# Kernel tuning notes

Measured on AMD Instinct MI355X. Metric: run time of the kernel, lower is better.

The kernel has to match this reference:

```python
import jax, jax.numpy as jnp
from jax import lax
import numpy as np

VOCAB = 32000
EMB = 256
UNITS = 1024
STEPS = 128
START_TOKEN = 1


def setup_inputs() -> dict:
    key = jax.random.key(0)
    ks = jax.random.split(key, 7)
    B, Hf, Wf, C = 32, 8, 25, 512
    s = 0.02
    return {
        "image_encoding": jax.random.normal(ks[0], (B, Hf, Wf, C), jnp.float32),
        "embedding": jax.random.normal(ks[1], (VOCAB, EMB), jnp.float32) * s,
        "lstm_kernel": jax.random.normal(ks[2], (EMB + C, 4 * UNITS), jnp.float32) * s,
        "lstm_rec_kernel": jax.random.normal(ks[3], (UNITS, 4 * UNITS), jnp.float32) * s,
        "lstm_bias": jnp.zeros((4 * UNITS,), jnp.float32),
        "proj_w": jax.random.normal(ks[4], (UNITS, VOCAB), jnp.float32) * s,
        "proj_b": jnp.zeros((VOCAB,), jnp.float32),
    }


def _lstm_cell(x, h, c, K, R, b):
    # Keras LSTMCell: gate order i, f, c, o; sigmoid gates, tanh cell.
    z = x @ K + h @ R + b  # [B, 4*UNITS]
    zi, zf, zc, zo = jnp.split(z, 4, axis=-1)
    i = jax.nn.sigmoid(zi)
    f = jax.nn.sigmoid(zf)
    o = jax.nn.sigmoid(zo)
    c_new = f * c + i * jnp.tanh(zc)
    h_new = o * jnp.tanh(c_new)
    return h_new, c_new


def reference(image_encoding, embedding, lstm_kernel, lstm_rec_kernel, lstm_bias, proj_w, proj_b):
    B = image_encoding.shape[0]
    C = image_encoding.shape[-1]
    # flatten_image_features=False -> mean over spatial positions
    features = image_encoding.reshape(B, -1, C).mean(axis=1)  # [B, C]

    start_emb = jnp.tile(embedding[START_TOKEN][None, :], (B, 1))  # [B, EMB]
    h0 = jnp.zeros((B, UNITS), features.dtype)
    c0 = jnp.zeros((B, UNITS), features.dtype)
    key0 = jax.random.key(42)

    def step(carry, _):
        h, c, inp, key = carry
        key, sub = jax.random.split(key)
        x = jnp.concatenate([inp, features], axis=-1)  # augment(inp)
        h, c = _lstm_cell(x, h, c, lstm_kernel, lstm_rec_kernel, lstm_bias)
        logits = h @ proj_w + proj_b  # [B, VOCAB]
        samples = jax.random.categorical(sub, logits)  # [B] int
        inp = embedding[samples]  # [B, EMB]
        return (h, c, inp, key), samples

    _, samples = lax.scan(step, (h0, c0, start_emb, key0), None, length=STEPS)
    # samples: [STEPS, B] -> [B, STEPS] as in tf.transpose(convert_to_tensor(output))
    return samples.T
```

## Files before the change

kernel.cpp:

```cpp
#include <hip/hip_runtime.h>
#include <cstdint>
#include <cstddef>


#define VOCAB 32000
#define EMB 256
#define UNITS 1024
#define STEPS 128
#define BATCH 32
#define XROWS 768
#define TINYF 1.17549435e-38f

typedef uint32_t u32x16 __attribute__((ext_vector_type(16)));

__host__ __device__ __forceinline__ void tf2x32(uint32_t k0, uint32_t k1,
                                                uint32_t x0, uint32_t x1,
                                                uint32_t& o0, uint32_t& o1) {
  uint32_t ks2 = k0 ^ k1 ^ 0x1BD11BDAu;
#define TFR(r) { x0 += x1; x1 = (x1 << (r)) | (x1 >> (32 - (r))); x1 ^= x0; }
  x0 += k0; x1 += k1;
  TFR(13) TFR(15) TFR(26) TFR(6)  x0 += k1;  x1 += ks2 + 1u;
  TFR(17) TFR(29) TFR(16) TFR(24) x0 += ks2; x1 += k0 + 2u;
  TFR(13) TFR(15) TFR(26) TFR(6)  x0 += k0;  x1 += k1 + 3u;
  TFR(17) TFR(29) TFR(16) TFR(24) x0 += k1;  x1 += ks2 + 4u;
  TFR(13) TFR(15) TFR(26) TFR(6)  x0 += ks2; x1 += k0 + 5u;
#undef TFR
  o0 = x0; o1 = x1;
}

__device__ __forceinline__ void sload2_b(const float* p, u32x16& a, u32x16& b,
                                         u32x16& c, u32x16& d) {
  asm volatile("s_load_dwordx16 %0, %4, 0x0\n\t"
               "s_load_dwordx16 %1, %4, 0x40\n\t"
               "s_load_dwordx16 %2, %4, 0x80\n\t"
               "s_load_dwordx16 %3, %4, 0xc0\n\t"
               "s_waitcnt lgkmcnt(0)"
               : "=&s"(a), "=&s"(b), "=&s"(c), "=&s"(d)
               : "s"(p));
}

__device__ __forceinline__ void fma32(float* acc, float w,
                                      const u32x16& xa, const u32x16& xb) {
#pragma unroll
  for (int b = 0; b < 16; ++b)
    acc[b] = fmaf(w, __uint_as_float(xa[b]), acc[b]);
#pragma unroll
  for (int b = 0; b < 16; ++b)
    acc[b + 16] = fmaf(w, __uint_as_float(xb[b]), acc[b + 16]);
}

__global__ __launch_bounds__(256) void k_init(
    const float* __restrict__ img, const float* __restrict__ emb,
    float* __restrict__ xT, float* __restrict__ h0, float* __restrict__ cT,
    unsigned long long* __restrict__ winners, unsigned int* __restrict__ cntA,
    unsigned int* __restrict__ cntB) {
  int idx = blockIdx.x * 256 + threadIdx.x;
  if (idx < 16384) {
    int b = idx >> 9, ch = idx & 511;
    const float* p = img + (size_t)b * 102400 + ch;
    float s = 0.f;
    for (int t = 0; t < 200; ++t) s += p[(size_t)t * 512];
    xT[(size_t)(256 + ch) * 32 + b] = s / 200.0f;
  } else if (idx < 24576) {
    int i2 = idx - 16384;
    int e = i2 >> 5, b = i2 & 31;
    xT[(size_t)e * 32 + b] = emb[256 + e];
  } else if (idx < 57344) {
    h0[idx - 24576] = 0.f;
  } else if (idx < 90112) {
    cT[idx - 57344] = 0.f;
  } else if (idx < 94208) {
    winners[idx - 90112] = 0ull;
  } else if (idx < 96256) {
    cntA[idx - 94208] = 0u;
  } else if (idx < 96384) {
    cntB[idx - 96256] = 0u;
  }
}

__global__ __launch_bounds__(512) void k_lstm(
    const float* __restrict__ Km, const float* __restrict__ Rm,
    const float* __restrict__ bias, const float* __restrict__ xT,
    const float* __restrict__ hr, float* __restrict__ hw,
    float* __restrict__ cT, float* __restrict__ zpart,
    unsigned int* cntA, int t) {
  const int tid = threadIdx.x;
  const int lane = tid & 63;
  const int strip = __builtin_amdgcn_readfirstlane(tid >> 6);
  const int jt = blockIdx.x >> 3;
  const int e = blockIdx.x & 7;
  const int j = jt * 64 + lane;
  const int m = jt & 15;

  __shared__ float red[4][64][33];
  __shared__ int lastf;

  float acc[32];
#pragma unroll
  for (int b = 0; b < 32; ++b) acc[b] = 0.f;

  const int klo = e * 224 + strip * 28;
  const int khi = klo + 28;

#define WROW(g) ((g) < XROWS ? Km[(size_t)(g) * 4096 + j] \
                             : Rm[(size_t)((g) - XROWS) * 4096 + j])
  float wc0 = WROW(klo);
  float wc1 = WROW(klo + 1);
  for (int k = klo; k < khi; k += 2) {
    float wn0 = 0.f, wn1 = 0.f;
    if (k + 2 < khi) { wn0 = WROW(k + 2); wn1 = WROW(k + 3); }
    const float* xrow = (k < XROWS) ? (xT + (size_t)k * 32)
                                    : (hr + (size_t)(k - XROWS) * 32);
    u32x16 xa, xb, xc, xd;
    sload2_b(xrow, xa, xb, xc, xd);
    fma32(acc, wc0, xa, xb);
    fma32(acc, wc1, xc, xd);
    wc0 = wn0; wc1 = wn1;
  }
#undef WROW

  if (strip < 4) {
#pragma unroll
    for (int b = 0; b < 32; ++b) red[strip][lane][b] = acc[b];
  }
  __syncthreads();
  if (strip >= 4) {
#pragma unroll
    for (int b = 0; b < 32; ++b) red[strip - 4][lane][b] += acc[b];
  }
  __syncthreads();

#pragma unroll
  for (int it = 0; it < 4; ++it) {
    int idx = it * 512 + tid;
    int col = idx >> 5, b = idx & 31;
    float s = ((red[0][col][b] + red[1][col][b]) + red[2][col][b]) +
              red[3][col][b];
    zpart[((size_t)e * 4096 + jt * 64 + col) * 32 + b] = s;
  }
  __syncthreads();
  if (tid == 0) {
    __threadfence();
    unsigned int old = atomicAdd(&cntA[t * 16 + m], 1u);
    lastf = (old == 31u);
  }
  __syncthreads();

  if (lastf) {
    __threadfence();
#pragma unroll
    for (int it = 0; it < 4; ++it) {
      int idx = it * 512 + tid;
      int ul = idx >> 5, b = idx & 31;
      int u = m * 64 + ul;
      float zs[4];
#pragma unroll
      for (int g = 0; g < 4; ++g) {
        int jj = g * 1024 + u;
        const float* zp = zpart + (size_t)jj * 32 + b;
        float s = zp[0];
#pragma unroll
        for (int ee = 1; ee < 8; ++ee) s += zp[(size_t)ee * 4096 * 32];
        zs[g] = s + bias[jj];
      }
      float ig = 1.0f / (1.0f + expf(-zs[0]));
      float fg = 1.0f / (1.0f + expf(-zs[1]));
      float og = 1.0f / (1.0f + expf(-zs[3]));
      float cold = cT[(size_t)u * 32 + b];
      float cn = fg * cold + ig * tanhf(zs[2]);
      cT[(size_t)u * 32 + b] = cn;
      hw[(size_t)u * 32 + b] = og * tanhf(cn);
    }
  }
}

__global__ __launch_bounds__(512) void k_logits(
    const float* __restrict__ Pw, const float* __restrict__ pb,
    const float* __restrict__ emb, const float* __restrict__ hr,
    float* __restrict__ xT, unsigned long long* winners,
    unsigned int* cntB, int* __restrict__ out, int t, uint32_t s0,
    uint32_t s1) {
  const int tid = threadIdx.x;
  const int lane = tid & 63;
  const int strip = __builtin_amdgcn_readfirstlane(tid >> 6);
  const int v0 = blockIdx.x * 64;

  __shared__ float red[4][64][33];
  __shared__ unsigned long long wbs[32][17];
  __shared__ int samp[BATCH];
  __shared__ int lastf;

  float acc[32];
#pragma unroll
  for (int b = 0; b < 32; ++b) acc[b] = 0.f;

  {
    const float* xp = hr + (size_t)(strip * 128) * 32;
    const float* wp = Pw + (size_t)(strip * 128) * VOCAB + v0 + lane;
    float wc0 = wp[0], wc1 = wp[VOCAB], wc2 = wp[2 * VOCAB],
          wc3 = wp[3 * VOCAB];
    const float* wpp = wp + (size_t)4 * VOCAB;
    u32x16 xa, xb, xc, xd;
    for (int k = 0; k < 124; k += 4) {
      float wn0 = wpp[0], wn1 = wpp[VOCAB], wn2 = wpp[2 * VOCAB],
            wn3 = wpp[3 * VOCAB];
      wpp += (size_t)4 * VOCAB;
      sload2_b(xp, xa, xb, xc, xd); xp += 64;
      fma32(acc, wc0, xa, xb);
      fma32(acc, wc1, xc, xd);
      sload2_b(xp, xa, xb, xc, xd); xp += 64;
      fma32(acc, wc2, xa, xb);
      fma32(acc, wc3, xc, xd);
      wc0 = wn0; wc1 = wn1; wc2 = wn2; wc3 = wn3;
    }
    sload2_b(xp, xa, xb, xc, xd); xp += 64;
    fma32(acc, wc0, xa, xb);
    fma32(acc, wc1, xc, xd);
    sload2_b(xp, xa, xb, xc, xd);
    fma32(acc, wc2, xa, xb);
    fma32(acc, wc3, xc, xd);
  }

  if (strip < 4) {
#pragma unroll
    for (int b = 0; b < 32; ++b) red[strip][lane][b] = acc[b];
  }
  __syncthreads();
  if (strip >= 4) {
#pragma unroll
    for (int b = 0; b < 32; ++b) red[strip - 4][lane][b] += acc[b];
  }
  __syncthreads();

#pragma unroll
  for (int it = 0; it < 4; ++it) {
    int idx = it * 512 + tid;
    int col = idx >> 5, b = idx & 31;
    float s = ((red[0][col][b] + red[1][col][b]) + red[2][col][b]) +
              red[3][col][b] + pb[v0 + col];
    red[0][col][b] = s;
  }
  __syncthreads();

  {
    const int b = tid & 31;
    const int sub = tid >> 5;
    unsigned long long best = 0ull;
#pragma unroll
    for (int c = 0; c < 4; ++c) {
      int col = sub * 4 + c;
      int vv = v0 + col;
      float logit = red[0][col][b];
      uint32_t y0, y1;
      tf2x32(s0, s1, 0u, (uint32_t)(b * VOCAB + vv), y0, y1);
      uint32_t bits = y0 ^ y1;
      uint32_t fb = (bits >> 9) | 0x3F800000u;
      float f = __uint_as_float(fb) - 1.0f;
      float u = f + TINYF;
      u = fmaxf(TINYF, u);
      float g = -logf(-logf(u));
      float val = g + logit;
      uint32_t ub = __float_as_uint(val);
      ub = ((int)ub < 0) ? ~ub : (ub | 0x80000000u);
      unsigned long long pk =
          ((unsigned long long)ub << 32) | (uint32_t)(~(uint32_t)vv);
      if (pk > best) best = pk;
    }
    wbs[b][sub] = best;
  }
  __syncthreads();

  if (tid < 32) {
    unsigned long long best = wbs[tid][0];
#pragma unroll
    for (int s = 1; s < 16; ++s)
      best = (wbs[tid][s] > best) ? wbs[tid][s] : best;
    unsigned long long cur = winners[t * 32 + tid];
    if (best > cur) atomicMax(&winners[t * 32 + tid], best);
  }
  __syncthreads();
  if (tid == 0) {
    __threadfence();
    unsigned int old = atomicAdd(&cntB[t], 1u);
    lastf = (old == 499u);
  }
  __syncthreads();

  if (lastf) {
    __threadfence();
    if (tid < 32) {
      unsigned long long w = atomicMax(&winners[t * 32 + tid], 0ull);
      int vv = (int)(~(uint32_t)(w & 0xFFFFFFFFull));
      samp[tid] = vv;
      out[tid * STEPS + t] = vv;
    }
    __syncthreads();
#pragma unroll
    for (int it = 0; it < 16; ++it) {
      int idx = it * 512 + tid;
      int b = idx >> 8, e2 = idx & 255;
      xT[(size_t)e2 * 32 + b] = emb[(size_t)samp[b] * EMB + e2];
    }
  }
}

extern "C" void kernel_launch(void* const* d_in, const int* in_sizes, int n_in,
                              void* d_out, int out_size, void* d_ws,
                              size_t ws_size, hipStream_t stream) {
  (void)in_sizes; (void)n_in; (void)out_size; (void)ws_size;
  const float* img  = (const float*)d_in[0];
  const float* emb  = (const float*)d_in[1];
  const float* Km   = (const float*)d_in[2];
  const float* Rm   = (const float*)d_in[3];
  const float* bias = (const float*)d_in[4];
  const float* Pw   = (const float*)d_in[5];
  const float* pb   = (const float*)d_in[6];
  int* out = (int*)d_out;

  char* ws = (char*)d_ws;
  unsigned long long* winners = (unsigned long long*)(ws + 0);
  unsigned int* cntA = (unsigned int*)(ws + 32768);
  unsigned int* cntB = (unsigned int*)(ws + 40960);
  float* xT   = (float*)(ws + 49152);
  float* hb0  = (float*)(ws + 147456);
  float* hb1  = (float*)(ws + 278528);
  float* cT   = (float*)(ws + 409600);
  float* zpart = (float*)(ws + 540672);

  k_init<<<377, 256, 0, stream>>>(img, emb, xT, hb0, cT, winners, cntA, cntB);

  uint32_t k0 = 0u, k1 = 42u;
  for (int t = 0; t < STEPS; ++t) {
    uint32_t n0, n1, su0, su1;
    tf2x32(k0, k1, 0u, 0u, n0, n1);
    tf2x32(k0, k1, 0u, 1u, su0, su1);
    k0 = n0; k1 = n1;

    const float* hrd = (t & 1) ? hb1 : hb0;
    float* hwr = (t & 1) ? hb0 : hb1;
    k_lstm<<<512, 512, 0, stream>>>(Km, Rm, bias, xT, hrd, hwr, cT, zpart,
                                    cntA, t);
    k_logits<<<500, 512, 0, stream>>>(Pw, pb, emb, hwr, xT, winners, cntB,
                                      out, t, su0, su1);
  }
}
```

Baseline: 11.22 ms.

## Split logits projection K-dimension across two blocks per vocab tile with atomic handoff

```diff
diff --git a/kernel.cpp b/kernel.cpp
--- a/kernel.cpp
+++ b/kernel.cpp
@@ -53,7 +53,7 @@
     const float* __restrict__ img, const float* __restrict__ emb,
     float* __restrict__ xT, float* __restrict__ h0, float* __restrict__ cT,
     unsigned long long* __restrict__ winners, unsigned int* __restrict__ cntA,
-    unsigned int* __restrict__ cntB) {
+    unsigned int* __restrict__ cntB, unsigned int* __restrict__ cntCD) {
   int idx = blockIdx.x * 256 + threadIdx.x;
   if (idx < 16384) {
     int b = idx >> 9, ch = idx & 511;
@@ -75,6 +75,8 @@
     cntA[idx - 94208] = 0u;
   } else if (idx < 96384) {
     cntB[idx - 96256] = 0u;
+  } else if (idx < 97384) {
+    cntCD[idx - 96384] = 0u;
   }
 }
 
@@ -178,30 +180,35 @@
     const float* __restrict__ Pw, const float* __restrict__ pb,
     const float* __restrict__ emb, const float* __restrict__ hr,
     float* __restrict__ xT, unsigned long long* winners,
-    unsigned int* cntB, int* __restrict__ out, int t, uint32_t s0,
+    unsigned int* cntB, unsigned int* cntC, unsigned int* doneF,
+    float* __restrict__ zlog, int* __restrict__ out, int t, uint32_t s0,
     uint32_t s1) {
   const int tid = threadIdx.x;
   const int lane = tid & 63;
   const int strip = __builtin_amdgcn_readfirstlane(tid >> 6);
-  const int v0 = blockIdx.x * 64;
+  const int tile = blockIdx.x >> 1;
+  const int half = blockIdx.x & 1;
+  const int v0 = tile * 64;
 
   __shared__ float red[4][64][33];
   __shared__ unsigned long long wbs[32][17];
   __shared__ int samp[BATCH];
   __shared__ int lastf;
+  __shared__ int roleS;
 
   float acc[32];
 #pragma unroll
   for (int b = 0; b < 32; ++b) acc[b] = 0.f;
 
   {
-    const float* xp = hr + (size_t)(strip * 128) * 32;
-    const float* wp = Pw + (size_t)(strip * 128) * VOCAB + v0 + lane;
+    const int r0 = half * 512 + strip * 64;
+    const float* xp = hr + (size_t)r0 * 32;
+    const float* wp = Pw + (size_t)r0 * VOCAB + v0 + lane;
     float wc0 = wp[0], wc1 = wp[VOCAB], wc2 = wp[2 * VOCAB],
           wc3 = wp[3 * VOCAB];
     const float* wpp = wp + (size_t)4 * VOCAB;
     u32x16 xa, xb, xc, xd;
-    for (int k = 0; k < 124; k += 4) {
+    for (int k = 0; k < 60; k += 4) {
       float wn0 = wpp[0], wn1 = wpp[VOCAB], wn2 = wpp[2 * VOCAB],
             wn3 = wpp[3 * VOCAB];
       wpp += (size_t)4 * VOCAB;
@@ -232,13 +239,45 @@
   }
   __syncthreads();
 
+  float sv[4];
 #pragma unroll
   for (int it = 0; it < 4; ++it) {
     int idx = it * 512 + tid;
     int col = idx >> 5, b = idx & 31;
-    float s = ((red[0][col][b] + red[1][col][b]) + red[2][col][b]) +
-              red[3][col][b] + pb[v0 + col];
-    red[0][col][b] = s;
+    sv[it] = ((red[0][col][b] + red[1][col][b]) + red[2][col][b]) +
+             red[3][col][b];
+  }
+
+  if (tid == 0) roleS = (int)(atomicAdd(&cntC[tile], 1u) & 1u);
+  __syncthreads();
+
+  float* zt = zlog + (size_t)tile * 2048;
+  if (roleS == 0) {
+#pragma unroll
+    for (int it = 0; it < 4; ++it) zt[it * 512 + tid] = sv[it];
+    __syncthreads();
+    if (tid == 0) {
+      __threadfence();
+      atomicAdd(&doneF[tile], 1u);
+    }
+    return;
+  }
+
+#pragma unroll
+  for (int it = 0; it < 4; ++it) {
+    int idx = it * 512 + tid;
+    red[0][idx >> 5][idx & 31] = sv[it];
+  }
+  if (tid == 0) {
+    while (atomicMax(&doneF[tile], 0u) < (unsigned)(t + 1)) {}
+  }
+  __syncthreads();
+  __threadfence();
+#pragma unroll
+  for (int it = 0; it < 4; ++it) {
+    int idx = it * 512 + tid;
+    int col = idx >> 5, b = idx & 31;
+    red[0][col][b] = (red[0][col][b] + zt[idx]) + pb[v0 + col];
   }
   __syncthreads();
 
@@ -321,13 +360,16 @@
   unsigned long long* winners = (unsigned long long*)(ws + 0);
   unsigned int* cntA = (unsigned int*)(ws + 32768);
   unsigned int* cntB = (unsigned int*)(ws + 40960);
+  unsigned int* cntC = (unsigned int*)(ws + 43008);
+  unsigned int* doneF = (unsigned int*)(ws + 45008);
   float* xT   = (float*)(ws + 49152);
   float* hb0  = (float*)(ws + 147456);
   float* hb1  = (float*)(ws + 278528);
   float* cT   = (float*)(ws + 409600);
   float* zpart = (float*)(ws + 540672);
 
-  k_init<<<377, 256, 0, stream>>>(img, emb, xT, hb0, cT, winners, cntA, cntB);
+  k_init<<<381, 256, 0, stream>>>(img, emb, xT, hb0, cT, winners, cntA, cntB,
+                                  cntC );
 
   uint32_t k0 = 0u, k1 = 42u;
   for (int t = 0; t < STEPS; ++t) {
@@ -340,7 +382,7 @@
     float* hwr = (t & 1) ? hb0 : hb1;
     k_lstm<<<512, 512, 0, stream>>>(Km, Rm, bias, xT, hrd, hwr, cT, zpart,
                                     cntA, t);
-    k_logits<<<500, 512, 0, stream>>>(Pw, pb, emb, hwr, xT, winners, cntB,
-                                      out, t, su0, su1);
-  }
-}
+    k_logits<<<1000, 512, 0, stream>>>(Pw, pb, emb, hwr, xT, winners, cntB,
+                                       cntC, doneF, zpart, out, t, su0, su1);
+  }
+}
```

After: 29.80 ms. 166% more time.

## Split batch across two blocks in LSTM and logits kernels

Applied to the files above, without the earlier changes.

```diff
diff --git a/kernel.cpp b/kernel.cpp
--- a/kernel.cpp
+++ b/kernel.cpp
@@ -28,25 +28,21 @@
   o0 = x0; o1 = x1;
 }
 
-__device__ __forceinline__ void sload2_b(const float* p, u32x16& a, u32x16& b,
-                                         u32x16& c, u32x16& d) {
+__device__ __forceinline__ void sload4h(const float* p, u32x16& a, u32x16& b,
+                                        u32x16& c, u32x16& d) {
   asm volatile("s_load_dwordx16 %0, %4, 0x0\n\t"
-               "s_load_dwordx16 %1, %4, 0x40\n\t"
-               "s_load_dwordx16 %2, %4, 0x80\n\t"
-               "s_load_dwordx16 %3, %4, 0xc0\n\t"
+               "s_load_dwordx16 %1, %4, 0x80\n\t"
+               "s_load_dwordx16 %2, %4, 0x100\n\t"
+               "s_load_dwordx16 %3, %4, 0x180\n\t"
                "s_waitcnt lgkmcnt(0)"
                : "=&s"(a), "=&s"(b), "=&s"(c), "=&s"(d)
                : "s"(p));
 }
 
-__device__ __forceinline__ void fma32(float* acc, float w,
-                                      const u32x16& xa, const u32x16& xb) {
+__device__ __forceinline__ void fma16(float* acc, float w, const u32x16& x) {
 #pragma unroll
   for (int b = 0; b < 16; ++b)
-    acc[b] = fmaf(w, __uint_as_float(xa[b]), acc[b]);
-#pragma unroll
-  for (int b = 0; b < 16; ++b)
-    acc[b + 16] = fmaf(w, __uint_as_float(xb[b]), acc[b + 16]);
+    acc[b] = fmaf(w, __uint_as_float(x[b]), acc[b]);
 }
 
 __global__ __launch_bounds__(256) void k_init(
@@ -87,17 +83,19 @@
   const int tid = threadIdx.x;
   const int lane = tid & 63;
   const int strip = __builtin_amdgcn_readfirstlane(tid >> 6);
-  const int jt = blockIdx.x >> 3;
-  const int e = blockIdx.x & 7;
+  const int bh = blockIdx.x & 1;
+  const int e = (blockIdx.x >> 1) & 7;
+  const int jt = blockIdx.x >> 4;
   const int j = jt * 64 + lane;
   const int m = jt & 15;
-
-  __shared__ float red[4][64][33];
+  const int b0 = bh * 16;
+
+  __shared__ float red[4][64][17];
   __shared__ int lastf;
 
-  float acc[32];
-#pragma unroll
-  for (int b = 0; b < 32; ++b) acc[b] = 0.f;
+  float acc[16];
+#pragma unroll
+  for (int b = 0; b < 16; ++b) acc[b] = 0.f;
 
   const int klo = e * 224 + strip * 28;
   const int khi = klo + 28;
@@ -106,43 +104,50 @@
                              : Rm[(size_t)((g) - XROWS) * 4096 + j])
   float wc0 = WROW(klo);
   float wc1 = WROW(klo + 1);
-  for (int k = klo; k < khi; k += 2) {
-    float wn0 = 0.f, wn1 = 0.f;
-    if (k + 2 < khi) { wn0 = WROW(k + 2); wn1 = WROW(k + 3); }
-    const float* xrow = (k < XROWS) ? (xT + (size_t)k * 32)
-                                    : (hr + (size_t)(k - XROWS) * 32);
+  float wc2 = WROW(klo + 2);
+  float wc3 = WROW(klo + 3);
+  for (int k = klo; k < khi; k += 4) {
+    float wn0 = 0.f, wn1 = 0.f, wn2 = 0.f, wn3 = 0.f;
+    if (k + 4 < khi) {
+      wn0 = WROW(k + 4); wn1 = WROW(k + 5);
+      wn2 = WROW(k + 6); wn3 = WROW(k + 7);
+    }
+    const float* xrow = ((k < XROWS) ? (xT + (size_t)k * 32)
+                                     : (hr + (size_t)(k - XROWS) * 32)) + b0;
     u32x16 xa, xb, xc, xd;
-    sload2_b(xrow, xa, xb, xc, xd);
-    fma32(acc, wc0, xa, xb);
-    fma32(acc, wc1, xc, xd);
-    wc0 = wn0; wc1 = wn1;
+    sload4h(xrow, xa, xb, xc, xd);
+    fma16(acc, wc0, xa);
+    fma16(acc, wc1, xb);
+    fma16(acc, wc2, xc);
+    fma16(acc, wc3, xd);
+    wc0 = wn0; wc1 = wn1; wc2 = wn2; wc3 = wn3;
   }
 #undef WROW
 
   if (strip < 4) {
 #pragma unroll
-    for (int b = 0; b < 32; ++b) red[strip][lane][b] = acc[b];
+    for (int b = 0; b < 16; ++b) red[strip][lane][b] = acc[b];
   }
   __syncthreads();
   if (strip >= 4) {
 #pragma unroll
-    for (int b = 0; b < 32; ++b) red[strip - 4][lane][b] += acc[b];
-  }
-  __syncthreads();
-
-#pragma unroll
-  for (int it = 0; it < 4; ++it) {
+    for (int b = 0; b < 16; ++b) red[strip - 4][lane][b] += acc[b];
+  }
+  __syncthreads();
+
+#pragma unroll
+  for (int it = 0; it < 2; ++it) {
     int idx = it * 512 + tid;
-    int col = idx >> 5, b = idx & 31;
-    float s = ((red[0][col][b] + red[1][col][b]) + red[2][col][b]) +
-              red[3][col][b];
-    zpart[((size_t)e * 4096 + jt * 64 + col) * 32 + b] = s;
+    int col = idx >> 4, bb = idx & 15;
+    float s = ((red[0][col][bb] + red[1][col][bb]) + red[2][col][bb]) +
+              red[3][col][bb];
+    zpart[((size_t)e * 4096 + jt * 64 + col) * 32 + b0 + bb] = s;
   }
   __syncthreads();
   if (tid == 0) {
     __threadfence();
     unsigned int old = atomicAdd(&cntA[t * 16 + m], 1u);
-    lastf = (old == 31u);
+    lastf = (old == 63u);
   }
   __syncthreads();
 
@@ -183,19 +188,22 @@
   const int tid = threadIdx.x;
   const int lane = tid & 63;
   const int strip = __builtin_amdgcn_readfirstlane(tid >> 6);
-  const int v0 = blockIdx.x * 64;
-
-  __shared__ float red[4][64][33];
-  __shared__ unsigned long long wbs[32][17];
+  const int tile = blockIdx.x >> 1;
+  const int bh = blockIdx.x & 1;
+  const int v0 = tile * 64;
+  const int b0 = bh * 16;
+
+  __shared__ float red[4][64][17];
+  __shared__ unsigned long long wbs[16][33];
   __shared__ int samp[BATCH];
   __shared__ int lastf;
 
-  float acc[32];
-#pragma unroll
-  for (int b = 0; b < 32; ++b) acc[b] = 0.f;
+  float acc[16];
+#pragma unroll
+  for (int b = 0; b < 16; ++b) acc[b] = 0.f;
 
   {
-    const float* xp = hr + (size_t)(strip * 128) * 32;
+    const float* xp = hr + (size_t)(strip * 128) * 32 + b0;
     const float* wp = Pw + (size_t)(strip * 128) * VOCAB + v0 + lane;
     float wc0 = wp[0], wc1 = wp[VOCAB], wc2 = wp[2 * VOCAB],
           wc3 = wp[3 * VOCAB];
@@ -205,54 +213,52 @@
       float wn0 = wpp[0], wn1 = wpp[VOCAB], wn2 = wpp[2 * VOCAB],
             wn3 = wpp[3 * VOCAB];
       wpp += (size_t)4 * VOCAB;
-      sload2_b(xp, xa, xb, xc, xd); xp += 64;
-      fma32(acc, wc0, xa, xb);
-      fma32(acc, wc1, xc, xd);
-      sload2_b(xp, xa, xb, xc, xd); xp += 64;
-      fma32(acc, wc2, xa, xb);
-      fma32(acc, wc3, xc, xd);
+      sload4h(xp, xa, xb, xc, xd); xp += 128;
+      fma16(acc, wc0, xa);
+      fma16(acc, wc1, xb);
+      fma16(acc, wc2, xc);
+      fma16(acc, wc3, xd);
       wc0 = wn0; wc1 = wn1; wc2 = wn2; wc3 = wn3;
     }
-    sload2_b(xp, xa, xb, xc, xd); xp += 64;
-    fma32(acc, wc0, xa, xb);
-    fma32(acc, wc1, xc, xd);
-    sload2_b(xp, xa, xb, xc, xd);
-    fma32(acc, wc2, xa, xb);
-    fma32(acc, wc3, xc, xd);
+    sload4h(xp, xa, xb, xc, xd);
+    fma16(acc, wc0, xa);
+    fma16(acc, wc1, xb);
+    fma16(acc, wc2, xc);
+    fma16(acc, wc3, xd);
   }
 
   if (strip < 4) {
 #pragma unroll
-    for (int b = 0; b < 32; ++b) red[strip][lane][b] = acc[b];
+    for (int b = 0; b < 16; ++b) red[strip][lane][b] = acc[b];
   }
   __syncthreads();
   if (strip >= 4) {
 #pragma unroll
-    for (int b = 0; b < 32; ++b) red[strip - 4][lane][b] += acc[b];
-  }
-  __syncthreads();
-
-#pragma unroll
-  for (int it = 0; it < 4; ++it) {
+    for (int b = 0; b < 16; ++b) red[strip - 4][lane][b] += acc[b];
+  }
+  __syncthreads();
+
+#pragma unroll
+  for (int it = 0; it < 2; ++it) {
     int idx = it * 512 + tid;
-    int col = idx >> 5, b = idx & 31;
-    float s = ((red[0][col][b] + red[1][col][b]) + red[2][col][b]) +
-              red[3][col][b] + pb[v0 + col];
-    red[0][col][b] = s;
+    int col = idx >> 4, bb = idx & 15;
+    float s = ((red[0][col][bb] + red[1][col][bb]) + red[2][col][bb]) +
+              red[3][col][bb] + pb[v0 + col];
+    red[0][col][bb] = s;
   }
   __syncthreads();
 
   {
-    const int b = tid & 31;
-    const int sub = tid >> 5;
+    const int b = tid & 15;
+    const int sub = tid >> 4;
     unsigned long long best = 0ull;
 #pragma unroll
-    for (int c = 0; c < 4; ++c) {
-      int col = sub * 4 + c;
+    for (int c = 0; c < 2; ++c) {
+      int col = sub * 2 + c;
       int vv = v0 + col;
       float logit = red[0][col][b];
       uint32_t y0, y1;
-      tf2x32(s0, s1, 0u, (uint32_t)(b * VOCAB + vv), y0, y1);
+      tf2x32(s0, s1, 0u, (uint32_t)((b0 + b) * VOCAB + vv), y0, y1);
       uint32_t bits = y0 ^ y1;
       uint32_t fb = (bits >> 9) | 0x3F800000u;
       float f = __uint_as_float(fb) - 1.0f;
@@ -270,19 +276,19 @@
   }
   __syncthreads();
 
-  if (tid < 32) {
+  if (tid < 16) {
     unsigned long long best = wbs[tid][0];
 #pragma unroll
-    for (int s = 1; s < 16; ++s)
+    for (int s = 1; s < 32; ++s)
       best = (wbs[tid][s] > best) ? wbs[tid][s] : best;
-    unsigned long long cur = winners[t * 32 + tid];
-    if (best > cur) atomicMax(&winners[t * 32 + tid], best);
+    unsigned long long cur = winners[t * 32 + b0 + tid];
+    if (best > cur) atomicMax(&winners[t * 32 + b0 + tid], best);
   }
   __syncthreads();
   if (tid == 0) {
     __threadfence();
     unsigned int old = atomicAdd(&cntB[t], 1u);
-    lastf = (old == 499u);
+    lastf = (old == 999u);
   }
   __syncthreads();
 
@@ -338,9 +344,9 @@
 
     const float* hrd = (t & 1) ? hb1 : hb0;
     float* hwr = (t & 1) ? hb0 : hb1;
-    k_lstm<<<512, 512, 0, stream>>>(Km, Rm, bias, xT, hrd, hwr, cT, zpart,
-                                    cntA, t);
-    k_logits<<<500, 512, 0, stream>>>(Pw, pb, emb, hwr, xT, winners, cntB,
-                                      out, t, su0, su1);
-  }
-}
+    k_lstm<<<1024, 512, 0, stream>>>(Km, Rm, bias, xT, hrd, hwr, cT, zpart,
+                                     cntA, t);
+    k_logits<<<1000, 512, 0, stream>>>(Pw, pb, emb, hwr, xT, winners, cntB,
+                                       out, t, su0, su1);
+  }
+}
```

Result: slower. 18.31 ms (+63.2%).
